# Optimization experiments

Measured on AMD Instinct MI355X. Metric: run time of the kernel, lower is better.

Reference implementation:

```python
import jax, jax.numpy as jnp
import numpy as np

Q_DIM, T_DIM, TOP_M, TEMP = 512, 768, 5, 0.07
B, H, W, K = 8, 64, 64, 128
LN_EPS = 1e-5

def _layernorm(x, g, b):
    mu = jnp.mean(x, axis=-1, keepdims=True)
    var = jnp.mean(jnp.square(x - mu), axis=-1, keepdims=True)
    return (x - mu) * jax.lax.rsqrt(var + LN_EPS) * g + b

def _l2norm(x):
    n = jnp.linalg.norm(x, axis=-1, keepdims=True)
    return x / jnp.maximum(n, 1e-12)

def setup_inputs() -> dict:
    key = jax.random.key(0)
    ks = jax.random.split(key, 12)
    s = lambda d: 1.0 / np.sqrt(d)
    return {
        'visual_features': jax.random.normal(ks[0], (B, H, W, Q_DIM), jnp.float32),
        'text_features': jax.random.normal(ks[1], (B, K, T_DIM), jnp.float32),
        'Wq': jax.random.uniform(ks[2], (Q_DIM, T_DIM), jnp.float32, -s(Q_DIM), s(Q_DIM)),
        'bq': jnp.zeros((T_DIM,), jnp.float32),
        'Wv': jax.random.uniform(ks[3], (T_DIM, Q_DIM), jnp.float32, -s(T_DIM), s(T_DIM)),
        'bv': jnp.zeros((Q_DIM,), jnp.float32),
        'W1': jax.random.uniform(ks[4], (Q_DIM, 4 * Q_DIM), jnp.float32, -s(Q_DIM), s(Q_DIM)),
        'b1': jnp.zeros((4 * Q_DIM,), jnp.float32),
        'W2': jax.random.uniform(ks[5], (4 * Q_DIM, Q_DIM), jnp.float32, -s(4 * Q_DIM), s(4 * Q_DIM)),
        'b2': jnp.zeros((Q_DIM,), jnp.float32),
        'g1': jnp.ones((Q_DIM,), jnp.float32), 'be1': jnp.zeros((Q_DIM,), jnp.float32),
        'g2': jnp.ones((Q_DIM,), jnp.float32), 'be2': jnp.zeros((Q_DIM,), jnp.float32),
    }

def reference(visual_features, text_features, Wq, bq, Wv, bv, W1, b1, W2, b2, g1, be1, g2, be2):
    b, h, w, c = visual_features.shape
    residual = visual_features.reshape(b, h * w, c)
    vis = _layernorm(residual, g1, be1)                      # (B,N,C)
    query = _l2norm(vis @ Wq + bq)                            # (B,N,Ct)
    keyt = _l2norm(text_features)                             # (B,K,Ct)
    value = text_features @ Wv + bv                           # (B,K,C)
    sim = jnp.einsum('bnc,bkc->bnk', query, keyt)             # (B,N,K)
    # top-M sparsification: keep top_m logits, others -> -inf
    top_v = jax.lax.top_k(sim, TOP_M)[0]                      # (B,N,M) sorted desc
    thr = top_v[..., -1:]
    sim = jnp.where(sim >= thr, sim, -jnp.inf)
    attn = jax.nn.softmax(sim / TEMP, axis=-1)
    aligned = jnp.einsum('bnk,bkc->bnc', attn, value)
    fused = residual + aligned
    fused = _layernorm(fused, g2, be2)
    ffn = jax.nn.gelu(fused @ W1 + b1, approximate=False) @ W2 + b2
    out = fused + ffn
    return out.reshape(b, h, w, c)
```

## Files before the change

kernel.cpp:

```cpp
#include <hip/hip_runtime.h>
#include <math.h>

typedef unsigned short u16;
typedef unsigned int   u32;
typedef unsigned long long u64;
typedef __attribute__((ext_vector_type(4))) float f32x4;
typedef __attribute__((ext_vector_type(4))) unsigned int u32x4;
typedef __attribute__((ext_vector_type(8))) _Float16 f16x8;
typedef __attribute__((ext_vector_type(8))) short s16x8;

#define NROWS   32768
#define CDIM    512
#define TDIM    768
#define KKEY    128
#define FFDIM   2048
#define NB      8
#define RPB     4096
#define LN_EPS_ 1e-5f
#define TINV    (1.0f/0.07f)
#define RESCUE_MARGIN 1e-5f

__device__ __forceinline__ u16 f2h(float f){ _Float16 h=(_Float16)f; return __builtin_bit_cast(u16,h); }
__device__ __forceinline__ float h2f(u16 v){ return (float)__builtin_bit_cast(_Float16, v); }
__device__ __forceinline__ unsigned pk2(float a,float b){ return (unsigned)f2h(a)|((unsigned)f2h(b)<<16); }
__device__ __forceinline__ u16 f2b(float f){
  u32 u = __builtin_bit_cast(u32, f);
  u32 r = (u + 0x7fffu + ((u>>16)&1u)) >> 16;
  return (u16)r;
}
__device__ __forceinline__ float b2f(u16 h){ u32 u = ((u32)h)<<16; return __builtin_bit_cast(float, u); }
__device__ __forceinline__ unsigned pkb(float a,float b){ return (unsigned)f2b(a)|((unsigned)f2b(b)<<16); }

__device__ __forceinline__ void gl_lds16(const void* g, void* l){
  __builtin_amdgcn_global_load_lds(
      (const __attribute__((address_space(1))) u32*)g,
      (__attribute__((address_space(3))) u32*)l, 16, 0, 0);
}

__device__ __forceinline__ float fast_exp2(float x){
#if __has_builtin(__builtin_amdgcn_exp2f)
  return __builtin_amdgcn_exp2f(x);
#else
  return exp2f(x);
#endif
}
__device__ __forceinline__ float fast_rcp(float x){
#if __has_builtin(__builtin_amdgcn_rcpf)
  return __builtin_amdgcn_rcpf(x);
#else
  return 1.0f/x;
#endif
}

__device__ __forceinline__ float wsumf(float v){
#pragma unroll
  for(int o=1;o<64;o<<=1) v+=__shfl_xor(v,o);
  return v; }
__device__ __forceinline__ float wmaxf(float v){
#pragma unroll
  for(int o=1;o<64;o<<=1) v=fmaxf(v,__shfl_xor(v,o));
  return v; }
__device__ __forceinline__ double wsumd(double v){
#pragma unroll
  for(int o=1;o<64;o<<=1) v+=__shfl_xor(v,o);
  return v; }
__device__ __forceinline__ double wmaxd(double v){
#pragma unroll
  for(int o=1;o<64;o<<=1){ double t=__shfl_xor(v,o); v = t>v ? t : v; }
  return v; }

__device__ __forceinline__ double blocksumd4(double v, double* red){
  const int lane = threadIdx.x & 63, w = threadIdx.x >> 6;
  v = wsumd(v);
  __syncthreads();
  if (lane==0) red[w] = v;
  __syncthreads();
  return red[0]+red[1]+red[2]+red[3];
}

template<int R, int C, int MODE>
__device__ __forceinline__ void tr_tile(const float* __restrict__ in, void* __restrict__ out,
                                        int bx, int by, float (*tile)[33])
{
  int c0 = bx*32, r0 = by*32;
  int tx = threadIdx.x, ty = threadIdx.y;
#pragma unroll
  for (int i=0;i<4;i++){
    int r = r0 + ty + i*8;
    tile[ty+i*8][tx] = in[(size_t)r*C + c0 + tx];
  }
  __syncthreads();
#pragma unroll
  for (int i=0;i<4;i++){
    int cc = c0 + ty + i*8, rr = r0 + tx;
    float v = tile[tx][ty+i*8];
    if (MODE==1)      ((u16*)out)[(size_t)cc*R + rr] = f2h(v);
    else if (MODE==2) ((u16*)out)[(size_t)cc*R + rr] = f2b(v);
    else              ((float*)out)[(size_t)cc*R + rr] = v;
  }
}

__global__ __launch_bounds__(256) void transpose_all_kernel(
    const float* __restrict__ Wq, const float* __restrict__ W1,
    const float* __restrict__ W2, const float* __restrict__ Wv,
    u16* __restrict__ Wqbt, u16* __restrict__ W116t,
    u16* __restrict__ W216t, float* __restrict__ WvT)
{
  __shared__ float tile[32][33];
  int bid = blockIdx.x;
  if (bid < 384){
    tr_tile<512,768,2>(Wq, Wqbt, bid%24, bid/24, tile);
  } else if (bid < 1408){
    int b = bid-384;  tr_tile<512,2048,1>(W1, W116t, b%64, b/64, tile);
  } else if (bid < 2432){
    int b = bid-1408; tr_tile<2048,512,1>(W2, W216t, b%16, b/16, tile);
  } else {
    int b = bid-2432; tr_tile<768,512,0>(Wv, WvT, b%16, b/16, tile);
  }
}

__global__ __launch_bounds__(256) void keystats_kernel(
    const float* __restrict__ text, const float* __restrict__ bq,
    float* __restrict__ normk, float* __restrict__ crr)
{
  int gw = blockIdx.x*4 + (threadIdx.x>>6);
  int lane = threadIdx.x & 63;
  const float* tr = &text[(size_t)gw*TDIM];
  double ss=0.0, db=0.0;
#pragma unroll
  for (int i=0;i<12;i++){
    float v = tr[lane + 64*i];
    ss += (double)v*(double)v;
    db += (double)bq[lane+64*i]*(double)v;
  }
  ss = wsumd(ss); db = wsumd(db);
  if (lane==0){
    double nk = sqrt(ss); nk = nk>1e-12 ? nk : 1e-12;
    normk[gw] = (float)nk;
    crr[gw]   = (float)db;
  }
}

__global__ __launch_bounds__(256) void ln1_kernel(
    const float* __restrict__ visual, const float* __restrict__ g1, const float* __restrict__ be1,
    u16* __restrict__ visH, u16* __restrict__ visL)
{
  int row = blockIdx.x*4 + (threadIdx.x>>6);
  int lane = threadIdx.x & 63;
  size_t base = (size_t)row*CDIM + lane*8;
  f32x4 a = *(const f32x4*)&visual[base];
  f32x4 c = *(const f32x4*)&visual[base+4];
  float s = a[0]+a[1]+a[2]+a[3]+c[0]+c[1]+c[2]+c[3];
  s = wsumf(s);
  float mu = s * (1.0f/512.0f);
  float q = 0.f;
#pragma unroll
  for (int i=0;i<4;i++){ float d=a[i]-mu; q+=d*d; }
#pragma unroll
  for (int i=0;i<4;i++){ float d=c[i]-mu; q+=d*d; }
  q = wsumf(q);
  float rs = rsqrtf(q*(1.0f/512.0f) + LN_EPS_);
  int cb = lane*8;
  float o[8];
#pragma unroll
  for (int i=0;i<4;i++) o[i]   = (a[i]-mu)*rs*g1[cb+i]   + be1[cb+i];
#pragma unroll
  for (int i=0;i<4;i++) o[4+i] = (c[i]-mu)*rs*g1[cb+4+i] + be1[cb+4+i];
  u16 hh[8];
  float lo[8];
#pragma unroll
  for (int i=0;i<8;i++){ hh[i] = f2b(o[i]); lo[i] = o[i] - b2f(hh[i]); }
  u32x4 hv, lv;
#pragma unroll
  for (int i=0;i<4;i++){
    hv[i] = (u32)hh[2*i] | ((u32)hh[2*i+1]<<16);
    lv[i] = pkb(lo[2*i], lo[2*i+1]);
  }
  *(u32x4*)&visH[base] = hv;
  *(u32x4*)&visL[base] = lv;
}

__global__ __launch_bounds__(256) void gemm_f32_kernel(
    const float* __restrict__ A, const float* __restrict__ Bt, float* __restrict__ C,
    int M, int N, int K, long sA, long sB, long sC)
{
  __shared__ float As[64][17];
  __shared__ float Bs[64][17];
  const int z = blockIdx.z;
  A  += (size_t)z * sA; Bt += (size_t)z * sB; C += (size_t)z * sC;
  const int tid = threadIdx.x;
  const int tx = tid & 15, ty = tid >> 4;
  const int m0 = blockIdx.x*64, n0 = blockIdx.y*64;
  float acc[4][4];
#pragma unroll
  for (int i=0;i<4;i++)
#pragma unroll
    for (int j=0;j<4;j++) acc[i][j]=0.f;
  const int lr = tid >> 2, lc = (tid & 3)*4;
  for (int k0=0; k0<K; k0+=16){
    f32x4 av = *(const f32x4*)&A [(size_t)(m0+lr)*K + k0 + lc];
    f32x4 bv = *(const f32x4*)&Bt[(size_t)(n0+lr)*K + k0 + lc];
#pragma unroll
    for (int i=0;i<4;i++){ As[lr][lc+i]=av[i]; Bs[lr][lc+i]=bv[i]; }
    __syncthreads();
#pragma unroll
    for (int kk=0; kk<16; kk++){
      float a[4], b[4];
#pragma unroll
      for (int i=0;i<4;i++){ a[i]=As[ty*4+i][kk]; b[i]=Bs[tx*4+i][kk]; }
#pragma unroll
      for (int i=0;i<4;i++)
#pragma unroll
        for (int j=0;j<4;j++) acc[i][j] = fmaf(a[i], b[j], acc[i][j]);
    }
    __syncthreads();
  }
#pragma unroll
  for (int i=0;i<4;i++){
    f32x4 o;
#pragma unroll
    for (int j=0;j<4;j++) o[j]=acc[i][j];
    *(f32x4*)&C[(size_t)(m0+ty*4+i)*N + n0 + tx*4] = o;
  }
}

__global__ __launch_bounds__(256) void split_kernel(
    const float* __restrict__ in, u16* __restrict__ hi, u16* __restrict__ lo, int n4)
{
  int i = blockIdx.x*256 + threadIdx.x;
  if (i >= n4) return;
  f32x4 v = *(const f32x4*)&in[i*4];
  u32 hw[2], lw[2];
#pragma unroll
  for (int j=0;j<2;j++){
    u16 h0 = f2b(v[2*j]), h1 = f2b(v[2*j+1]);
    hw[j] = (u32)h0 | ((u32)h1<<16);
    lw[j] = pkb(v[2*j]-b2f(h0), v[2*j+1]-b2f(h1));
  }
  ((u32*)hi)[i*2]   = hw[0]; ((u32*)hi)[i*2+1] = hw[1];
  ((u32*)lo)[i*2]   = lw[0]; ((u32*)lo)[i*2+1] = lw[1];
}

__device__ __forceinline__ float gelu_exact(float v){
  float x  = v*0.70710678118654752440f;
  float ax = fabsf(x);
  float t  = fast_rcp(fmaf(0.3275911f, ax, 1.0f));
  float p  = t*fmaf(t, fmaf(t, fmaf(t, fmaf(t, 1.061405429f, -1.453152027f),
                  1.421413741f), -0.284496736f), 0.254829592f);
  float e  = fast_exp2(ax*ax*(-1.4426950408889634f));
  float y  = 1.0f - p*e;
  float er = (x < 0.0f) ? -y : y;
  return 0.5f*v*(1.0f + er);
}

template<int EPI, int NN, int KK, int NT>
__global__ __launch_bounds__(256) void gemm_f16_kernel(
    const u16* __restrict__ A, const u16* __restrict__ Bt,
    const float* __restrict__ bias,
    float* __restrict__ out_f,
    u16* __restrict__ out_h,
    const u16* __restrict__ add_h)
{
  __shared__ __align__(16) u16 As[2][128*64];
  __shared__ __align__(16) u16 Bs[2][128*64];
  const int tid = threadIdx.x;
  const int lane = tid & 63, w = tid >> 6;
  const int wr = w >> 1, wc = w & 1;
  constexpr int NWG = 256*NT;
  const int wg = blockIdx.x;
  const int b2 = (wg & 7)*(NWG/8) + (wg >> 3);
  const int ntile = b2 % NT, mtile = b2 / NT;
  const int m0 = mtile*128, n0 = ntile*128;
  f32x4 acc[4][4];
#pragma unroll
  for (int i=0;i<4;i++)
#pragma unroll
    for (int j=0;j<4;j++) acc[i][j] = (f32x4)0.f;
  const int lr = lane & 15, lk = (lane >> 4)*8;
  const int c8_sw = ((lane & 7) ^ (lane >> 3))*8;
  const size_t stride32 = (size_t)32*KK;
  const u16* aBase = &A [(size_t)(m0 + w*8 + (lane>>3))*KK + c8_sw];
  const u16* bBase = &Bt[(size_t)(n0 + w*8 + (lane>>3))*KK + c8_sw];

  auto STAGE = [&](int buf, int k0){
#pragma unroll
    for (int i=0;i<4;i++){
      gl_lds16(aBase + i*stride32 + k0, &As[buf][w*512 + i*2048]);
      gl_lds16(bBase + i*stride32 + k0, &Bs[buf][w*512 + i*2048]);
    }
  };

  STAGE(0, 0);
  int cur = 0;
  for (int k0=0; k0<KK; k0+=64){
    if (k0 + 64 < KK){
      STAGE(cur^1, k0+64);
      asm volatile("s_waitcnt vmcnt(8)" ::: "memory");
    } else {
      asm volatile("s_waitcnt vmcnt(0)" ::: "memory");
    }
    __builtin_amdgcn_s_barrier();
#pragma unroll
    for (int kk=0; kk<64; kk+=32){
      s16x8 af[4], bfv[4];
      const int csw = (kk + lk) ^ ((lr & 7) << 3);
#pragma unroll
      for (int mi=0;mi<4;mi++) af[mi]  = *(const s16x8*)&As[cur][(wr*64 + mi*16 + lr)*64 + csw];
#pragma unroll
      for (int ni=0;ni<4;ni++) bfv[ni] = *(const s16x8*)&Bs[cur][(wc*64 + ni*16 + lr)*64 + csw];
#pragma unroll
      for (int mi=0;mi<4;mi++)
#pragma unroll
        for (int ni=0;ni<4;ni++){
          if (EPI == 0)
            acc[mi][ni] = __builtin_amdgcn_mfma_f32_16x16x32_bf16(af[mi], bfv[ni], acc[mi][ni], 0, 0, 0);
          else
            acc[mi][ni] = __builtin_amdgcn_mfma_f32_16x16x32_f16(
                __builtin_bit_cast(f16x8, af[mi]), __builtin_bit_cast(f16x8, bfv[ni]), acc[mi][ni], 0, 0, 0);
        }
    }
    __builtin_amdgcn_s_barrier();
    cur ^= 1;
  }
  const int lr4 = (lane >> 4)*4;
  if (EPI == 0){
    float sq[4][4];
#pragma unroll
    for (int mi=0;mi<4;mi++)
#pragma unroll
      for (int r=0;r<4;r++) sq[mi][r]=0.f;
#pragma unroll
    for (int ni=0;ni<4;ni++){
      float bqv = bias[n0 + wc*64 + ni*16 + lr];
#pragma unroll
      for (int mi=0;mi<4;mi++)
#pragma unroll
        for (int r=0;r<4;r++){
          float v = acc[mi][ni][r] + bqv;
          sq[mi][r] += v*v;
        }
    }
#pragma unroll
    for (int o=1;o<16;o<<=1)
#pragma unroll
      for (int mi=0;mi<4;mi++)
#pragma unroll
        for (int r=0;r<4;r++) sq[mi][r] += __shfl_xor(sq[mi][r], o);
    if ((lane & 15) == 0){
      int part = ntile*2 + wc;
#pragma unroll
      for (int mi=0;mi<4;mi++)
#pragma unroll
        for (int r=0;r<4;r++){
          int row = m0 + wr*64 + mi*16 + lr4 + r;
          out_f[(size_t)row*12 + part] = sq[mi][r];
        }
    }
  } else {
    const int row0 = m0 + wr*64 + lr4;
    const int col0 = n0 + wc*64 + lr;
    float bb[4];
#pragma unroll
    for (int ni=0;ni<4;ni++) bb[ni] = bias[col0 + ni*16];
    if (EPI == 1){
      u16* op = out_h + (size_t)row0*NN + col0;
#pragma unroll
      for (int mi=0;mi<4;mi++)
#pragma unroll
        for (int r=0;r<4;r++)
#pragma unroll
          for (int ni=0;ni<4;ni++)
            op[(size_t)(mi*16+r)*NN + ni*16] = f2h(gelu_exact(acc[mi][ni][r] + bb[ni]));
    } else {
      float* op = out_f + (size_t)row0*NN + col0;
      const u16* rp = add_h + (size_t)row0*NN + col0;
#pragma unroll
      for (int mi=0;mi<4;mi++)
#pragma unroll
        for (int r=0;r<4;r++)
#pragma unroll
          for (int ni=0;ni<4;ni++)
            op[(size_t)(mi*16+r)*NN + ni*16] =
                acc[mi][ni][r] + bb[ni] + h2f(rp[(size_t)(mi*16+r)*NN + ni*16]);
    }
  }
}

__global__ __launch_bounds__(256) void gemm_t_kernel(
    const u16* __restrict__ Ah, const u16* __restrict__ Al,
    const u16* __restrict__ Bh, const u16* __restrict__ Bl,
    float* __restrict__ C)
{
  __shared__ __align__(16) u16 As[2][128*64];
  __shared__ __align__(16) u16 Bs[2][128*64];
  const int tid = threadIdx.x;
  const int lane = tid & 63, w = tid >> 6;
  const int wr = w >> 1, wc = w & 1;
  const int mtile = blockIdx.x;
  const int m0 = mtile*128, z = mtile >> 5;
  f32x4 acc[4][4];
#pragma unroll
  for (int i=0;i<4;i++)
#pragma unroll
    for (int j=0;j<4;j++) acc[i][j] = (f32x4)0.f;
  const int lr = lane & 15, lk = (lane >> 4)*8;
  const int c8_sw = ((lane & 7) ^ (lane >> 3))*8;
  const size_t aOff = (size_t)(m0 + w*8 + (lane>>3))*CDIM + c8_sw;
  const size_t bOff = (size_t)(z*KKEY + w*8 + (lane>>3))*CDIM + c8_sw;
  const size_t stride32 = (size_t)32*CDIM;

  auto STAGE = [&](int buf, int s){
    const int p = s >> 3, k0 = (s & 7) << 6;
    const u16* Ap = (p==2) ? Al : Ah;
    const u16* Bp = (p==1) ? Bl : Bh;
#pragma unroll
    for (int i=0;i<4;i++){
      gl_lds16(Ap + aOff + i*stride32 + k0, &As[buf][w*512 + i*2048]);
      gl_lds16(Bp + bOff + i*stride32 + k0, &Bs[buf][w*512 + i*2048]);
    }
  };

  STAGE(0, 0);
  int cur = 0;
  for (int s=0; s<24; ++s){
    if (s < 23){
      STAGE(cur^1, s+1);
      asm volatile("s_waitcnt vmcnt(8)" ::: "memory");
    } else {
      asm volatile("s_waitcnt vmcnt(0)" ::: "memory");
    }
    __builtin_amdgcn_s_barrier();
#pragma unroll
    for (int kk=0; kk<64; kk+=32){
      s16x8 af[4], bfv[4];
      const int csw = (kk + lk) ^ ((lr & 7) << 3);
#pragma unroll
      for (int mi=0;mi<4;mi++) af[mi]  = *(const s16x8*)&As[cur][(wr*64 + mi*16 + lr)*64 + csw];
#pragma unroll
      for (int ni=0;ni<4;ni++) bfv[ni] = *(const s16x8*)&Bs[cur][(wc*64 + ni*16 + lr)*64 + csw];
#pragma unroll
      for (int mi=0;mi<4;mi++)
#pragma unroll
        for (int ni=0;ni<4;ni++)
          acc[mi][ni] = __builtin_amdgcn_mfma_f32_16x16x32_bf16(af[mi], bfv[ni], acc[mi][ni], 0, 0, 0);
    }
    __builtin_amdgcn_s_barrier();
    cur ^= 1;
  }
  const int lr4 = (lane >> 4)*4;
  const int row0 = m0 + wr*64 + lr4;
  const int col0 = wc*64 + lr;
  float* op = C + (size_t)row0*KKEY + col0;
#pragma unroll
  for (int mi=0;mi<4;mi++)
#pragma unroll
    for (int r=0;r<4;r++)
#pragma unroll
      for (int ni=0;ni<4;ni++)
        op[(size_t)(mi*16+r)*KKEY + ni*16] = acc[mi][ni][r];
}

__global__ __launch_bounds__(256) void rescue_kernel(
    const int* __restrict__ rcnt, const int* __restrict__ rlist,
    const float* __restrict__ visual, const float* __restrict__ text,
    const float* __restrict__ Wq, const float* __restrict__ bq,
    const float* __restrict__ g1, const float* __restrict__ be1,
    const float* __restrict__ g2, const float* __restrict__ be2,
    const float* __restrict__ value, const float* __restrict__ bv,
    u16* __restrict__ fused16)
{
  __shared__ double vis64[512];
  __shared__ double q64[768];
  __shared__ double sims[128];
  __shared__ double pw[128];
  __shared__ double red[4];
  __shared__ double sc2[2];
  __shared__ int klist[128];
  __shared__ int kcount;
  const int tid = threadIdx.x, lane = tid & 63, w = tid >> 6;
  int n = *rcnt; if (n > NROWS) n = NROWS;
  for (int i = blockIdx.x; i < n; i += gridDim.x){
    const int row = rlist[i], b = row >> 12;
    const size_t rb = (size_t)row*CDIM;
    double x0 = (double)visual[rb+tid], x1 = (double)visual[rb+tid+256];
    double s = blocksumd4(x0+x1, red);
    double mu = s*(1.0/512.0);
    double d0 = x0-mu, d1 = x1-mu;
    double var = blocksumd4(d0*d0+d1*d1, red);
    double rs = 1.0/sqrt(var*(1.0/512.0) + 1e-5);
    vis64[tid]     = d0*rs*(double)g1[tid]     + (double)be1[tid];
    vis64[tid+256] = d1*rs*(double)g1[tid+256] + (double)be1[tid+256];
    __syncthreads();
    double qa0=(double)bq[tid], qa1=(double)bq[tid+256], qa2=(double)bq[tid+512];
#pragma unroll 4
    for (int c=0;c<CDIM;c++){
      double v = vis64[c];
      const float* wrow = &Wq[(size_t)c*TDIM];
      qa0 += v*(double)wrow[tid];
      qa1 += v*(double)wrow[tid+256];
      qa2 += v*(double)wrow[tid+512];
    }
    q64[tid]=qa0; q64[tid+256]=qa1; q64[tid+512]=qa2;
    double nq2 = blocksumd4(qa0*qa0+qa1*qa1+qa2*qa2, red);
    double nq = sqrt(nq2); if (nq < 1e-12) nq = 1e-12;
    __syncthreads();
    if (tid < KKEY){
      const float* trow = &text[((size_t)b*KKEY + tid)*TDIM];
      double dot=0.0, nk2=0.0;
#pragma unroll 8
      for (int j=0;j<TDIM;j++){
        double tv = (double)trow[j];
        dot += q64[j]*tv; nk2 += tv*tv;
      }
      double nk = sqrt(nk2); if (nk < 1e-12) nk = 1e-12;
      sims[tid] = dot/(nq*nk);
    }
    __syncthreads();
    if (w == 0){
      double v0=sims[lane], v1=sims[lane+64];
      bool rm0=false, rm1=false;
      double thr=0.0, smax=0.0;
      for (int it=0; it<5; ++it){
        double c0 = rm0 ? -1e300 : v0;
        double c1 = rm1 ? -1e300 : v1;
        double m = wmaxd(c0>c1 ? c0 : c1);
        if (it==0) smax = m;
        thr = m;
        bool h0 = (!rm0) && (v0==m);
        u64 k0 = __ballot(h0);
        if (k0){ if (lane == __ffsll(k0)-1) rm0 = true; }
        else {
          bool h1 = (!rm1) && (v1==m);
          u64 k1 = __ballot(h1);
          if (lane == __ffsll(k1)-1) rm1 = true;
        }
      }
      if (lane==0){ sc2[0]=smax; sc2[1]=thr; kcount=0; }
    }
    __syncthreads();
    const double smax = sc2[0], thr = sc2[1];
    double p = 0.0;
    if (tid < KKEY){
      double sv = sims[tid];
      p = (sv >= thr) ? exp((sv-smax)*(1.0/0.07)) : 0.0;
      pw[tid] = p;
      if (p > 0.0){ int pos = atomicAdd(&kcount, 1); klist[pos] = tid; }
    }
    double Z = blocksumd4(p, red);
    double zi = 1.0/Z;
    __syncthreads();
    double a0=(double)bv[tid], a1=(double)bv[tid+256];
    int kc = kcount;
    for (int ki=0; ki<kc; ++ki){
      int k = klist[ki];
      double wt = pw[k]*zi;
      const float* vr = &value[((size_t)b*KKEY + k)*CDIM];
      a0 += wt*(double)vr[tid];
      a1 += wt*(double)vr[tid+256];
    }
    double f0 = (double)visual[rb+tid]     + a0;
    double f1 = (double)visual[rb+tid+256] + a1;
    double fsum = blocksumd4(f0+f1, red);
    double fmu = fsum*(1.0/512.0);
    double e0=f0-fmu, e1=f1-fmu;
    double fvar = blocksumd4(e0*e0+e1*e1, red);
    double frs = 1.0/sqrt(fvar*(1.0/512.0) + 1e-5);
    fused16[rb+tid]     = f2h((float)(e0*frs*(double)g2[tid]     + (double)be2[tid]));
    fused16[rb+tid+256] = f2h((float)(e1*frs*(double)g2[tid+256] + (double)be2[tid+256]));
    __syncthreads();
  }
}

__global__ __launch_bounds__(256) void attn_ln2_kernel(
    const float* __restrict__ visual,
    const float* __restrict__ tbuf, const float* __restrict__ crr,
    const float* __restrict__ normk, const float* __restrict__ qpart,
    const float* __restrict__ value, const float* __restrict__ bv,
    const float* __restrict__ g2, const float* __restrict__ be2,
    u16* __restrict__ fused16,
    int* __restrict__ rcnt, int* __restrict__ rlist)
{
  const int w = threadIdx.x >> 6, lane = threadIdx.x & 63;
  const int row = blockIdx.x*4 + w;
  const int b = row >> 12;
  float nqp = (lane < 12) ? qpart[(size_t)row*12 + lane] : 0.f;
  float nq2 = wsumf(nqp);
  float nq = fmaxf(sqrtf(nq2), 1e-12f);
  const float* trow = &tbuf[(size_t)row*KKEY];
  float s0 = (trow[lane]    + crr[b*KKEY + lane])    / (nq*normk[b*KKEY + lane]);
  float s1 = (trow[lane+64] + crr[b*KKEY + lane+64]) / (nq*normk[b*KKEY + lane+64]);
  float v0=s0, v1=s1; bool rm0=false, rm1=false;
  float thr=0.f, smax=0.f, m6=0.f;
  for (int it=0; it<6; ++it){
    float c0 = rm0 ? -1e30f : v0;
    float c1 = rm1 ? -1e30f : v1;
    float m = wmaxf(fmaxf(c0,c1));
    if (it==0) smax = m;
    if (it<5){
      thr = m;
      bool h0 = (!rm0) && (v0==m);
      u64 k0 = __ballot(h0);
      if (k0){ if (lane == __ffsll(k0)-1) rm0 = true; }
      else {
        bool h1 = (!rm1) && (v1==m);
        u64 k1 = __ballot(h1);
        if (lane == __ffsll(k1)-1) rm1 = true;
      }
    } else m6 = m;
  }
  if ((thr - m6) < RESCUE_MARGIN){
    if (lane == 0){
      int p = atomicAdd(rcnt, 1);
      rlist[p] = row;
    }
    return;
  }
  float p0 = (s0>=thr) ? expf((s0-smax)*TINV) : 0.f;
  float p1 = (s1>=thr) ? expf((s1-smax)*TINV) : 0.f;
  float Z = wsumf(p0+p1);
  float zi = 1.f/Z;
  float accv[8];
#pragma unroll
  for (int j=0;j<8;j++) accv[j] = bv[lane*8+j];
  u64 mk0 = __ballot(p0>0.f);
  u64 mk1 = __ballot(p1>0.f);
  while (mk0){
    int l = __ffsll(mk0)-1; mk0 &= mk0-1;
    float wt = __shfl(p0, l)*zi;
    const f32x4* vr = (const f32x4*)&value[((size_t)b*KKEY + l)*CDIM + lane*8];
    f32x4 va = vr[0], vb = vr[1];
#pragma unroll
    for (int j=0;j<4;j++){ accv[j] += wt*va[j]; accv[4+j] += wt*vb[j]; }
  }
  while (mk1){
    int l = __ffsll(mk1)-1; mk1 &= mk1-1;
    float wt = __shfl(p1, l)*zi;
    const f32x4* vr = (const f32x4*)&value[((size_t)b*KKEY + l + 64)*CDIM + lane*8];
    f32x4 va = vr[0], vb = vr[1];
#pragma unroll
    for (int j=0;j<4;j++){ accv[j] += wt*va[j]; accv[4+j] += wt*vb[j]; }
  }
  size_t rb = (size_t)row*CDIM + lane*8;
  f32x4 r0v = *(const f32x4*)&visual[rb];
  f32x4 r1v = *(const f32x4*)&visual[rb+4];
  float f[8];
#pragma unroll
  for (int j=0;j<4;j++){ f[j]=r0v[j]+accv[j]; f[4+j]=r1v[j]+accv[4+j]; }
  float fs=0.f;
#pragma unroll
  for (int j=0;j<8;j++) fs += f[j];
  fs = wsumf(fs);
  float fmu = fs*(1.0f/512.0f);
  float fvv=0.f;
#pragma unroll
  for (int j=0;j<8;j++){ float d=f[j]-fmu; fvv+=d*d; }
  fvv = wsumf(fvv);
  float frs = rsqrtf(fvv*(1.0f/512.0f) + LN_EPS_);
  int cb = lane*8;
  f32x4 o0,o1;
#pragma unroll
  for (int j=0;j<4;j++) o0[j] = (f[j]-fmu)*frs*g2[cb+j]     + be2[cb+j];
#pragma unroll
  for (int j=0;j<4;j++) o1[j] = (f[4+j]-fmu)*frs*g2[cb+4+j] + be2[cb+4+j];
  u32x4 hv;
  hv[0]=pk2(o0[0],o0[1]); hv[1]=pk2(o0[2],o0[3]);
  hv[2]=pk2(o1[0],o1[1]); hv[3]=pk2(o1[2],o1[3]);
  *(u32x4*)&fused16[rb] = hv;
}

extern "C" void kernel_launch(void* const* d_in, const int* in_sizes, int n_in,
                              void* d_out, int out_size, void* d_ws, size_t ws_size,
                              hipStream_t stream)
{
  (void)in_sizes; (void)n_in; (void)out_size; (void)ws_size;
  const float* visual = (const float*)d_in[0];
  const float* text   = (const float*)d_in[1];
  const float* Wq     = (const float*)d_in[2];
  const float* bq     = (const float*)d_in[3];
  const float* Wv     = (const float*)d_in[4];
  const float* bv     = (const float*)d_in[5];
  const float* W1     = (const float*)d_in[6];
  const float* b1     = (const float*)d_in[7];
  const float* W2     = (const float*)d_in[8];
  const float* b2     = (const float*)d_in[9];
  const float* g1     = (const float*)d_in[10];
  const float* be1    = (const float*)d_in[11];
  const float* g2     = (const float*)d_in[12];
  const float* be2    = (const float*)d_in[13];
  float* out = (float*)d_out;

  char* ws = (char*)d_ws;
  size_t off = 0;
  auto alloc = [&](size_t bytes)->char*{
    char* p = ws + off; off += (bytes + 255) & ~(size_t)255; return p; };

  u16*    visH   = (u16*)   alloc((size_t)NROWS*CDIM*2);
  u16*    visL   = (u16*)   alloc((size_t)NROWS*CDIM*2);
  u16*    h16    = (u16*)   alloc((size_t)NROWS*FFDIM*2);
  u16*    fused16= (u16*)   alloc((size_t)NROWS*CDIM*2);
  float*  tbuf   = (float*) alloc((size_t)NROWS*KKEY*4);
  float*  Mrt    = (float*) alloc((size_t)NB*KKEY*CDIM*4);
  u16*    MrtH   = (u16*)   alloc((size_t)NB*KKEY*CDIM*2);
  u16*    MrtL   = (u16*)   alloc((size_t)NB*KKEY*CDIM*2);
  float*  value  = (float*) alloc((size_t)NB*KKEY*CDIM*4);
  u16*    Wqbt   = (u16*)   alloc((size_t)TDIM*CDIM*2);
  u16*    W116t  = (u16*)   alloc((size_t)FFDIM*CDIM*2);
  u16*    W216t  = (u16*)   alloc((size_t)CDIM*FFDIM*2);
  float*  WvT    = (float*) alloc((size_t)CDIM*TDIM*4);
  float*  qpart  = (float*) alloc((size_t)NROWS*12*4);
  float*  normk  = (float*) alloc((size_t)NB*KKEY*4);
  float*  crr    = (float*) alloc((size_t)NB*KKEY*4);
  int*    rcnt   = (int*)   alloc(256);
  int*    rlist  = (int*)   alloc((size_t)NROWS*4);

  hipMemsetAsync(rcnt, 0, sizeof(int), stream);

  transpose_all_kernel<<<2816, dim3(32,8), 0, stream>>>(
      Wq, W1, W2, Wv, Wqbt, W116t, W216t, WvT);
  keystats_kernel<<<256, 256, 0, stream>>>(text, bq, normk, crr);
  gemm_f32_kernel<<<dim3(2, 8, 8), 256, 0, stream>>>(
      text, Wq, Mrt, KKEY, CDIM, TDIM, (long)KKEY*TDIM, 0, (long)KKEY*CDIM);
  gemm_f32_kernel<<<dim3(2, 8, 8), 256, 0, stream>>>(
      text, WvT, value, KKEY, CDIM, TDIM, (long)KKEY*TDIM, 0, (long)KKEY*CDIM);
  split_kernel<<<512, 256, 0, stream>>>(Mrt, MrtH, MrtL, NB*KKEY*CDIM/4);
  ln1_kernel<<<NROWS/4, 256, 0, stream>>>(visual, g1, be1, visH, visL);
  gemm_t_kernel<<<256, 256, 0, stream>>>(visH, visL, MrtH, MrtL, tbuf);
  gemm_f16_kernel<0,TDIM,CDIM,6><<<1536, 256, 0, stream>>>(
      visH, Wqbt, bq, qpart, nullptr, nullptr);
  attn_ln2_kernel<<<NROWS/4, 256, 0, stream>>>(
      visual, tbuf, crr, normk, qpart, value, bv, g2, be2,
      fused16, rcnt, rlist);
  rescue_kernel<<<256, 256, 0, stream>>>(
      rcnt, rlist, visual, text, Wq, bq, g1, be1, g2, be2, value, bv, fused16);
  gemm_f16_kernel<1,FFDIM,CDIM,16><<<4096, 256, 0, stream>>>(
      fused16, W116t, b1, nullptr, h16, nullptr);
  gemm_f16_kernel<2,CDIM,FFDIM,4><<<1024, 256, 0, stream>>>(
      h16, W216t, b2, out, nullptr, fused16);
}
```

Baseline: 514.7 us.

## Use 256x256 tile 512-thread GEMM kernel for both FFN matmuls

Adds a new GEMM kernel with 256x256 output tiles, 8 waves per block and an XCD-aware block remap, used for both FFN matmuls in place of the 128x128 tile kernel. The larger tile raises arithmetic intensity per LDS load and cuts global traffic for A and B. The cost is more registers per wave (8x4 accumulators) and one block per CU, so latency hiding is reduced. The FFN2 GEMM now launches only 256 blocks, which may underfill the device.

New measurement: 526.1 us. +2.2%, slower.

```diff
diff --git a/kernel.cpp b/kernel.cpp
--- a/kernel.cpp
+++ b/kernel.cpp
@@ -356,33 +356,101 @@
           out_f[(size_t)row*12 + part] = sq[mi][r];
         }
     }
+  }
+}
+
+template<int EPI, int NN, int KK, int NT>
+__global__ __launch_bounds__(512, 1) void gemm_big_kernel(
+    const u16* __restrict__ A, const u16* __restrict__ Bt,
+    const float* __restrict__ bias,
+    float* __restrict__ out_f,
+    u16* __restrict__ out_h,
+    const u16* __restrict__ add_h)
+{
+  __shared__ __align__(16) u16 As[2][256*64];
+  __shared__ __align__(16) u16 Bs[2][256*64];
+  const int tid = threadIdx.x;
+  const int lane = tid & 63, w = tid >> 6;
+  const int wr = w >> 2, wc = w & 3;
+  constexpr int NWG = 128*NT;
+  const int wg = blockIdx.x;
+  const int b2 = (wg & 7)*(NWG/8) + (wg >> 3);
+  const int ntile = b2 % NT, mtile = b2 / NT;
+  const int m0 = mtile*256, n0 = ntile*256;
+  f32x4 acc[8][4];
+#pragma unroll
+  for (int i=0;i<8;i++)
+#pragma unroll
+    for (int j=0;j<4;j++) acc[i][j] = (f32x4)0.f;
+  const int lr = lane & 15, lk = (lane >> 4)*8;
+  const int c8_sw = ((lane & 7) ^ (lane >> 3))*8;
+  const size_t stride64 = (size_t)64*KK;
+  const u16* aBase = &A [(size_t)(m0 + w*8 + (lane>>3))*KK + c8_sw];
+  const u16* bBase = &Bt[(size_t)(n0 + w*8 + (lane>>3))*KK + c8_sw];
+
+  auto STAGE = [&](int buf, int k0){
+#pragma unroll
+    for (int i=0;i<4;i++){
+      gl_lds16(aBase + i*stride64 + k0, &As[buf][w*512 + i*4096]);
+      gl_lds16(bBase + i*stride64 + k0, &Bs[buf][w*512 + i*4096]);
+    }
+  };
+
+  STAGE(0, 0);
+  int cur = 0;
+  for (int k0=0; k0<KK; k0+=64){
+    if (k0 + 64 < KK){
+      STAGE(cur^1, k0+64);
+      asm volatile("s_waitcnt vmcnt(8)" ::: "memory");
+    } else {
+      asm volatile("s_waitcnt vmcnt(0)" ::: "memory");
+    }
+    __builtin_amdgcn_s_barrier();
+    __builtin_amdgcn_s_setprio(1);
+#pragma unroll
+    for (int kk=0; kk<64; kk+=32){
+      f16x8 af[8], bfv[4];
+      const int csw = (kk + lk) ^ ((lr & 7) << 3);
+#pragma unroll
+      for (int mi=0;mi<8;mi++) af[mi]  = *(const f16x8*)&As[cur][(wr*128 + mi*16 + lr)*64 + csw];
+#pragma unroll
+      for (int ni=0;ni<4;ni++) bfv[ni] = *(const f16x8*)&Bs[cur][(wc*64 + ni*16 + lr)*64 + csw];
+#pragma unroll
+      for (int mi=0;mi<8;mi++)
+#pragma unroll
+        for (int ni=0;ni<4;ni++)
+          acc[mi][ni] = __builtin_amdgcn_mfma_f32_16x16x32_f16(af[mi], bfv[ni], acc[mi][ni], 0, 0, 0);
+    }
+    __builtin_amdgcn_s_setprio(0);
+    __builtin_amdgcn_s_barrier();
+    cur ^= 1;
+  }
+  const int lr4 = (lane >> 4)*4;
+  const int row0 = m0 + wr*128 + lr4;
+  const int col0 = n0 + wc*64 + lr;
+  float bb[4];
+#pragma unroll
+  for (int ni=0;ni<4;ni++) bb[ni] = bias[col0 + ni*16];
+  if (EPI == 1){
+    u16* op = out_h + (size_t)row0*NN + col0;
+#pragma unroll
+    for (int mi=0;mi<8;mi++)
+#pragma unroll
+      for (int r=0;r<4;r++)
+#pragma unroll
+        for (int ni=0;ni<4;ni++)
+          op[(size_t)(mi*16+r)*NN + ni*16] = f2h(gelu_exact(acc[mi][ni][r] + bb[ni]));
   } else {
-    const int row0 = m0 + wr*64 + lr4;
-    const int col0 = n0 + wc*64 + lr;
-    float bb[4];
-#pragma unroll
-    for (int ni=0;ni<4;ni++) bb[ni] = bias[col0 + ni*16];
-    if (EPI == 1){
-      u16* op = out_h + (size_t)row0*NN + col0;
-#pragma unroll
-      for (int mi=0;mi<4;mi++)
-#pragma unroll
-        for (int r=0;r<4;r++)
-#pragma unroll
-          for (int ni=0;ni<4;ni++)
-            op[(size_t)(mi*16+r)*NN + ni*16] = f2h(gelu_exact(acc[mi][ni][r] + bb[ni]));
-    } else {
-      float* op = out_f + (size_t)row0*NN + col0;
-      const u16* rp = add_h + (size_t)row0*NN + col0;
-#pragma unroll
-      for (int mi=0;mi<4;mi++)
-#pragma unroll
-        for (int r=0;r<4;r++)
-#pragma unroll
-          for (int ni=0;ni<4;ni++)
-            op[(size_t)(mi*16+r)*NN + ni*16] =
-                acc[mi][ni][r] + bb[ni] + h2f(rp[(size_t)(mi*16+r)*NN + ni*16]);
-    }
+    float* op = out_f + (size_t)row0*NN + col0;
+    const u16* rp = add_h + (size_t)row0*NN + col0;
+#pragma unroll
+    for (int mi=0;mi<8;mi++)
+#pragma unroll
+      for (int r=0;r<4;r++)
+#pragma unroll
+        for (int ni=0;ni<4;ni++)
+          op[(size_t)(mi*16+r)*NN + ni*16] =
+              acc[mi][ni][r] + bb[ni] + h2f(rp[(size_t)(mi*16+r)*NN + ni*16]);
   }
 }
 
@@ -732,8 +800,8 @@
       fused16, rcnt, rlist);
   rescue_kernel<<<256, 256, 0, stream>>>(
       rcnt, rlist, visual, text, Wq, bq, g1, be1, g2, be2, value, bv, fused16);
-  gemm_f16_kernel<1,FFDIM,CDIM,16><<<4096, 256, 0, stream>>>(
+  gemm_big_kernel<1,FFDIM,CDIM,8><<<1024, 512, 0, stream>>>(
       fused16, W116t, b1, nullptr, h16, nullptr);
-  gemm_f16_kernel<2,CDIM,FFDIM,4><<<1024, 256, 0, stream>>>(
+  gemm_big_kernel<2,CDIM,FFDIM,2><<<256, 512, 0, stream>>>(
       h16, W216t, b2, out, nullptr, fused16);
 }
```

## Enlarge f16 GEMM tiles to 256x256 with 8 waves and prioritized MFMA phases

Applied to the files above, without the earlier changes.

Replaces the 128x128, 4-wave GEMM with a 256x256, 8-wave variant: each wave now computes a 128x64 sub-tile, and B fragments are held across four A sub-steps. The compute loop is split into phases with extra barriers and s_setprio around the MFMA bursts, so waves interleave LDS loads and matrix math. The aim is more reuse per byte loaded and fewer global loads per FLOP for the Q-projection, FFN1 and FFN2 GEMMs. In exchange, LDS use doubles to 128KB and register pressure grows, which forces one block per CU. The grids also get small: the FFN2 GEMM launches only 256 blocks, which may underfill the device.

After: 553.7 us. 1.08x slower.

```diff
diff --git a/kernel.cpp b/kernel.cpp
--- a/kernel.cpp
+++ b/kernel.cpp
@@ -254,39 +254,39 @@
 }
 
 template<int EPI, int NN, int KK, int NT>
-__global__ __launch_bounds__(256) void gemm_f16_kernel(
+__global__ __launch_bounds__(512, 1) void gemm_big_kernel(
     const u16* __restrict__ A, const u16* __restrict__ Bt,
     const float* __restrict__ bias,
     float* __restrict__ out_f,
     u16* __restrict__ out_h,
     const u16* __restrict__ add_h)
 {
-  __shared__ __align__(16) u16 As[2][128*64];
-  __shared__ __align__(16) u16 Bs[2][128*64];
+  __shared__ __align__(16) u16 As[2][256*64];
+  __shared__ __align__(16) u16 Bs[2][256*64];
   const int tid = threadIdx.x;
   const int lane = tid & 63, w = tid >> 6;
-  const int wr = w >> 1, wc = w & 1;
-  constexpr int NWG = 256*NT;
+  const int wr = w >> 2, wc = w & 3;
+  constexpr int NWG = 128*NT;
   const int wg = blockIdx.x;
   const int b2 = (wg & 7)*(NWG/8) + (wg >> 3);
   const int ntile = b2 % NT, mtile = b2 / NT;
-  const int m0 = mtile*128, n0 = ntile*128;
-  f32x4 acc[4][4];
-#pragma unroll
-  for (int i=0;i<4;i++)
+  const int m0 = mtile*256, n0 = ntile*256;
+  f32x4 acc[8][4];
+#pragma unroll
+  for (int i=0;i<8;i++)
 #pragma unroll
     for (int j=0;j<4;j++) acc[i][j] = (f32x4)0.f;
   const int lr = lane & 15, lk = (lane >> 4)*8;
   const int c8_sw = ((lane & 7) ^ (lane >> 3))*8;
-  const size_t stride32 = (size_t)32*KK;
+  const size_t stride64 = (size_t)64*KK;
   const u16* aBase = &A [(size_t)(m0 + w*8 + (lane>>3))*KK + c8_sw];
   const u16* bBase = &Bt[(size_t)(n0 + w*8 + (lane>>3))*KK + c8_sw];
 
   auto STAGE = [&](int buf, int k0){
 #pragma unroll
     for (int i=0;i<4;i++){
-      gl_lds16(aBase + i*stride32 + k0, &As[buf][w*512 + i*2048]);
-      gl_lds16(bBase + i*stride32 + k0, &Bs[buf][w*512 + i*2048]);
+      gl_lds16(aBase + i*stride64 + k0, &As[buf][w*512 + i*4096]);
+      gl_lds16(bBase + i*stride64 + k0, &Bs[buf][w*512 + i*4096]);
     }
   };
 
@@ -300,40 +300,57 @@
       asm volatile("s_waitcnt vmcnt(0)" ::: "memory");
     }
     __builtin_amdgcn_s_barrier();
-#pragma unroll
-    for (int kk=0; kk<64; kk+=32){
-      s16x8 af[4], bfv[4];
-      const int csw = (kk + lk) ^ ((lr & 7) << 3);
-#pragma unroll
-      for (int mi=0;mi<4;mi++) af[mi]  = *(const s16x8*)&As[cur][(wr*64 + mi*16 + lr)*64 + csw];
-#pragma unroll
-      for (int ni=0;ni<4;ni++) bfv[ni] = *(const s16x8*)&Bs[cur][(wc*64 + ni*16 + lr)*64 + csw];
-#pragma unroll
-      for (int mi=0;mi<4;mi++)
-#pragma unroll
-        for (int ni=0;ni<4;ni++){
-          if (EPI == 0)
-            acc[mi][ni] = __builtin_amdgcn_mfma_f32_16x16x32_bf16(af[mi], bfv[ni], acc[mi][ni], 0, 0, 0);
-          else
-            acc[mi][ni] = __builtin_amdgcn_mfma_f32_16x16x32_f16(
-                __builtin_bit_cast(f16x8, af[mi]), __builtin_bit_cast(f16x8, bfv[ni]), acc[mi][ni], 0, 0, 0);
+    s16x8 bfv[4][2];
+#pragma unroll
+    for (int ni=0;ni<4;ni++)
+#pragma unroll
+      for (int kh=0;kh<2;kh++){
+        const int csw = (kh*32 + lk) ^ ((lr & 7) << 3);
+        bfv[ni][kh] = *(const s16x8*)&Bs[cur][(wc*64 + ni*16 + lr)*64 + csw];
+      }
+#pragma unroll
+    for (int q=0;q<4;q++){
+      s16x8 af[2][2];
+#pragma unroll
+      for (int m2=0;m2<2;m2++)
+#pragma unroll
+        for (int kh=0;kh<2;kh++){
+          const int csw = (kh*32 + lk) ^ ((lr & 7) << 3);
+          af[m2][kh] = *(const s16x8*)&As[cur][(wr*128 + (q*2+m2)*16 + lr)*64 + csw];
         }
-    }
-    __builtin_amdgcn_s_barrier();
+      __builtin_amdgcn_s_barrier();
+      __builtin_amdgcn_s_setprio(1);
+#pragma unroll
+      for (int m2=0;m2<2;m2++)
+#pragma unroll
+        for (int ni=0;ni<4;ni++)
+#pragma unroll
+          for (int kh=0;kh<2;kh++){
+            if (EPI == 0)
+              acc[q*2+m2][ni] = __builtin_amdgcn_mfma_f32_16x16x32_bf16(
+                  af[m2][kh], bfv[ni][kh], acc[q*2+m2][ni], 0, 0, 0);
+            else
+              acc[q*2+m2][ni] = __builtin_amdgcn_mfma_f32_16x16x32_f16(
+                  __builtin_bit_cast(f16x8, af[m2][kh]),
+                  __builtin_bit_cast(f16x8, bfv[ni][kh]), acc[q*2+m2][ni], 0, 0, 0);
+          }
+      __builtin_amdgcn_s_setprio(0);
+      __builtin_amdgcn_s_barrier();
+    }
     cur ^= 1;
   }
   const int lr4 = (lane >> 4)*4;
   if (EPI == 0){
-    float sq[4][4];
-#pragma unroll
-    for (int mi=0;mi<4;mi++)
+    float sq[8][4];
+#pragma unroll
+    for (int mi=0;mi<8;mi++)
 #pragma unroll
       for (int r=0;r<4;r++) sq[mi][r]=0.f;
 #pragma unroll
     for (int ni=0;ni<4;ni++){
       float bqv = bias[n0 + wc*64 + ni*16 + lr];
 #pragma unroll
-      for (int mi=0;mi<4;mi++)
+      for (int mi=0;mi<8;mi++)
 #pragma unroll
         for (int r=0;r<4;r++){
           float v = acc[mi][ni][r] + bqv;
@@ -343,21 +360,21 @@
 #pragma unroll
     for (int o=1;o<16;o<<=1)
 #pragma unroll
-      for (int mi=0;mi<4;mi++)
+      for (int mi=0;mi<8;mi++)
 #pragma unroll
         for (int r=0;r<4;r++) sq[mi][r] += __shfl_xor(sq[mi][r], o);
     if ((lane & 15) == 0){
-      int part = ntile*2 + wc;
-#pragma unroll
-      for (int mi=0;mi<4;mi++)
+      int part = ntile*4 + wc;
+#pragma unroll
+      for (int mi=0;mi<8;mi++)
 #pragma unroll
         for (int r=0;r<4;r++){
-          int row = m0 + wr*64 + mi*16 + lr4 + r;
+          int row = m0 + wr*128 + mi*16 + lr4 + r;
           out_f[(size_t)row*12 + part] = sq[mi][r];
         }
     }
   } else {
-    const int row0 = m0 + wr*64 + lr4;
+    const int row0 = m0 + wr*128 + lr4;
     const int col0 = n0 + wc*64 + lr;
     float bb[4];
 #pragma unroll
@@ -365,7 +382,7 @@
     if (EPI == 1){
       u16* op = out_h + (size_t)row0*NN + col0;
 #pragma unroll
-      for (int mi=0;mi<4;mi++)
+      for (int mi=0;mi<8;mi++)
 #pragma unroll
         for (int r=0;r<4;r++)
 #pragma unroll
@@ -375,7 +392,7 @@
       float* op = out_f + (size_t)row0*NN + col0;
       const u16* rp = add_h + (size_t)row0*NN + col0;
 #pragma unroll
-      for (int mi=0;mi<4;mi++)
+      for (int mi=0;mi<8;mi++)
 #pragma unroll
         for (int r=0;r<4;r++)
 #pragma unroll
@@ -725,15 +742,15 @@
   split_kernel<<<512, 256, 0, stream>>>(Mrt, MrtH, MrtL, NB*KKEY*CDIM/4);
   ln1_kernel<<<NROWS/4, 256, 0, stream>>>(visual, g1, be1, visH, visL);
   gemm_t_kernel<<<256, 256, 0, stream>>>(visH, visL, MrtH, MrtL, tbuf);
-  gemm_f16_kernel<0,TDIM,CDIM,6><<<1536, 256, 0, stream>>>(
+  gemm_big_kernel<0,TDIM,CDIM,3><<<384, 512, 0, stream>>>(
       visH, Wqbt, bq, qpart, nullptr, nullptr);
   attn_ln2_kernel<<<NROWS/4, 256, 0, stream>>>(
       visual, tbuf, crr, normk, qpart, value, bv, g2, be2,
       fused16, rcnt, rlist);
   rescue_kernel<<<256, 256, 0, stream>>>(
       rcnt, rlist, visual, text, Wq, bq, g1, be1, g2, be2, value, bv, fused16);
-  gemm_f16_kernel<1,FFDIM,CDIM,16><<<4096, 256, 0, stream>>>(
+  gemm_big_kernel<1,FFDIM,CDIM,8><<<1024, 512, 0, stream>>>(
       fused16, W116t, b1, nullptr, h16, nullptr);
-  gemm_f16_kernel<2,CDIM,FFDIM,4><<<1024, 256, 0, stream>>>(
+  gemm_big_kernel<2,CDIM,FFDIM,2><<<256, 512, 0, stream>>>(
       h16, W216t, b2, out, nullptr, fused16);
 }
```

## Split similarity GEMM passes across blocks and fuse text GEMMs with hi/lo split

Applied to the files above, without the earlier changes.

The three hi/lo precision passes of the similarity GEMM now run as separate blocks (grid y=3), each writing its own partial buffer, and the attention kernel sums the three partials. This raises the GEMM from 256 blocks to 768 so more of the GPU is occupied. The cost is extra partial-buffer traffic, and the buffers alias the FFN hidden buffer h16, which is not yet in use at that point. The two small text GEMMs and the split kernel are merged into one launch that writes the bf16 hi/lo halves directly, removing two launches and an fp32 intermediate.

New measurement: 458.6 us. 10.9% less time.

```diff
diff --git a/kernel.cpp b/kernel.cpp
--- a/kernel.cpp
+++ b/kernel.cpp
@@ -180,14 +180,18 @@
   *(u32x4*)&visL[base] = lv;
 }
 
-__global__ __launch_bounds__(256) void gemm_f32_kernel(
-    const float* __restrict__ A, const float* __restrict__ Bt, float* __restrict__ C,
-    int M, int N, int K, long sA, long sB, long sC)
+__global__ __launch_bounds__(256) void gemm_txt_kernel(
+    const float* __restrict__ text, const float* __restrict__ Wq,
+    const float* __restrict__ WvT,
+    u16* __restrict__ MrtH, u16* __restrict__ MrtL, float* __restrict__ value)
 {
   __shared__ float As[64][17];
   __shared__ float Bs[64][17];
-  const int z = blockIdx.z;
-  A  += (size_t)z * sA; Bt += (size_t)z * sB; C += (size_t)z * sC;
+  const int zz = blockIdx.z;
+  const bool isV = zz >= 8;
+  const int z = isV ? zz-8 : zz;
+  const float* A  = text + (size_t)z*KKEY*TDIM;
+  const float* Bt = isV ? WvT : Wq;
   const int tid = threadIdx.x;
   const int tx = tid & 15, ty = tid >> 4;
   const int m0 = blockIdx.x*64, n0 = blockIdx.y*64;
@@ -197,9 +201,9 @@
 #pragma unroll
     for (int j=0;j<4;j++) acc[i][j]=0.f;
   const int lr = tid >> 2, lc = (tid & 3)*4;
-  for (int k0=0; k0<K; k0+=16){
-    f32x4 av = *(const f32x4*)&A [(size_t)(m0+lr)*K + k0 + lc];
-    f32x4 bv = *(const f32x4*)&Bt[(size_t)(n0+lr)*K + k0 + lc];
+  for (int k0=0; k0<TDIM; k0+=16){
+    f32x4 av = *(const f32x4*)&A [(size_t)(m0+lr)*TDIM + k0 + lc];
+    f32x4 bv = *(const f32x4*)&Bt[(size_t)(n0+lr)*TDIM + k0 + lc];
 #pragma unroll
     for (int i=0;i<4;i++){ As[lr][lc+i]=av[i]; Bs[lr][lc+i]=bv[i]; }
     __syncthreads();
@@ -217,28 +221,27 @@
   }
 #pragma unroll
   for (int i=0;i<4;i++){
-    f32x4 o;
-#pragma unroll
-    for (int j=0;j<4;j++) o[j]=acc[i][j];
-    *(f32x4*)&C[(size_t)(m0+ty*4+i)*N + n0 + tx*4] = o;
-  }
-}
-
-__global__ __launch_bounds__(256) void split_kernel(
-    const float* __restrict__ in, u16* __restrict__ hi, u16* __restrict__ lo, int n4)
-{
-  int i = blockIdx.x*256 + threadIdx.x;
-  if (i >= n4) return;
-  f32x4 v = *(const f32x4*)&in[i*4];
-  u32 hw[2], lw[2];
-#pragma unroll
-  for (int j=0;j<2;j++){
-    u16 h0 = f2b(v[2*j]), h1 = f2b(v[2*j+1]);
-    hw[j] = (u32)h0 | ((u32)h1<<16);
-    lw[j] = pkb(v[2*j]-b2f(h0), v[2*j+1]-b2f(h1));
-  }
-  ((u32*)hi)[i*2]   = hw[0]; ((u32*)hi)[i*2+1] = hw[1];
-  ((u32*)lo)[i*2]   = lw[0]; ((u32*)lo)[i*2+1] = lw[1];
+    size_t idx = ((size_t)z*KKEY + m0 + ty*4 + i)*CDIM + n0 + tx*4;
+    if (isV){
+      f32x4 o;
+#pragma unroll
+      for (int j=0;j<4;j++) o[j]=acc[i][j];
+      *(f32x4*)&value[idx] = o;
+    } else {
+      u16 hh[4]; u16 ll[4];
+#pragma unroll
+      for (int j=0;j<4;j++){
+        float v = acc[i][j];
+        u16 h = f2b(v);
+        hh[j] = h;
+        ll[j] = f2b(v - b2f(h));
+      }
+      ((u32*)&MrtH[idx])[0] = (u32)hh[0] | ((u32)hh[1]<<16);
+      ((u32*)&MrtH[idx])[1] = (u32)hh[2] | ((u32)hh[3]<<16);
+      ((u32*)&MrtL[idx])[0] = (u32)ll[0] | ((u32)ll[1]<<16);
+      ((u32*)&MrtL[idx])[1] = (u32)ll[2] | ((u32)ll[3]<<16);
+    }
+  }
 }
 
 __device__ __forceinline__ float gelu_exact(float v){
@@ -397,7 +400,10 @@
   const int lane = tid & 63, w = tid >> 6;
   const int wr = w >> 1, wc = w & 1;
   const int mtile = blockIdx.x;
+  const int p = blockIdx.y;
   const int m0 = mtile*128, z = mtile >> 5;
+  const u16* Ap = (p==2) ? Al : Ah;
+  const u16* Bp = (p==1) ? Bl : Bh;
   f32x4 acc[4][4];
 #pragma unroll
   for (int i=0;i<4;i++)
@@ -410,9 +416,7 @@
   const size_t stride32 = (size_t)32*CDIM;
 
   auto STAGE = [&](int buf, int s){
-    const int p = s >> 3, k0 = (s & 7) << 6;
-    const u16* Ap = (p==2) ? Al : Ah;
-    const u16* Bp = (p==1) ? Bl : Bh;
+    const int k0 = s << 6;
 #pragma unroll
     for (int i=0;i<4;i++){
       gl_lds16(Ap + aOff + i*stride32 + k0, &As[buf][w*512 + i*2048]);
@@ -422,8 +426,8 @@
 
   STAGE(0, 0);
   int cur = 0;
-  for (int s=0; s<24; ++s){
-    if (s < 23){
+  for (int s=0; s<8; ++s){
+    if (s < 7){
       STAGE(cur^1, s+1);
       asm volatile("s_waitcnt vmcnt(8)" ::: "memory");
     } else {
@@ -450,7 +454,7 @@
   const int lr4 = (lane >> 4)*4;
   const int row0 = m0 + wr*64 + lr4;
   const int col0 = wc*64 + lr;
-  float* op = C + (size_t)row0*KKEY + col0;
+  float* op = C + (size_t)p*NROWS*KKEY + (size_t)row0*KKEY + col0;
 #pragma unroll
   for (int mi=0;mi<4;mi++)
 #pragma unroll
@@ -586,9 +590,13 @@
   float nqp = (lane < 12) ? qpart[(size_t)row*12 + lane] : 0.f;
   float nq2 = wsumf(nqp);
   float nq = fmaxf(sqrtf(nq2), 1e-12f);
-  const float* trow = &tbuf[(size_t)row*KKEY];
-  float s0 = (trow[lane]    + crr[b*KKEY + lane])    / (nq*normk[b*KKEY + lane]);
-  float s1 = (trow[lane+64] + crr[b*KKEY + lane+64]) / (nq*normk[b*KKEY + lane+64]);
+  const float* t0 = &tbuf[(size_t)row*KKEY];
+  const float* t1 = t0 + (size_t)NROWS*KKEY;
+  const float* t2 = t1 + (size_t)NROWS*KKEY;
+  float ta = t0[lane]    + t1[lane]    + t2[lane];
+  float tb = t0[lane+64] + t1[lane+64] + t2[lane+64];
+  float s0 = (ta + crr[b*KKEY + lane])    / (nq*normk[b*KKEY + lane]);
+  float s1 = (tb + crr[b*KKEY + lane+64]) / (nq*normk[b*KKEY + lane+64]);
   float v0=s0, v1=s1; bool rm0=false, rm1=false;
   float thr=0.f, smax=0.f, m6=0.f;
   for (int it=0; it<6; ++it){
@@ -698,8 +706,6 @@
   u16*    visL   = (u16*)   alloc((size_t)NROWS*CDIM*2);
   u16*    h16    = (u16*)   alloc((size_t)NROWS*FFDIM*2);
   u16*    fused16= (u16*)   alloc((size_t)NROWS*CDIM*2);
-  float*  tbuf   = (float*) alloc((size_t)NROWS*KKEY*4);
-  float*  Mrt    = (float*) alloc((size_t)NB*KKEY*CDIM*4);
   u16*    MrtH   = (u16*)   alloc((size_t)NB*KKEY*CDIM*2);
   u16*    MrtL   = (u16*)   alloc((size_t)NB*KKEY*CDIM*2);
   float*  value  = (float*) alloc((size_t)NB*KKEY*CDIM*4);
@@ -712,19 +718,17 @@
   float*  crr    = (float*) alloc((size_t)NB*KKEY*4);
   int*    rcnt   = (int*)   alloc(256);
   int*    rlist  = (int*)   alloc((size_t)NROWS*4);
+  float*  tbuf   = (float*)h16;
 
   hipMemsetAsync(rcnt, 0, sizeof(int), stream);
 
   transpose_all_kernel<<<2816, dim3(32,8), 0, stream>>>(
       Wq, W1, W2, Wv, Wqbt, W116t, W216t, WvT);
   keystats_kernel<<<256, 256, 0, stream>>>(text, bq, normk, crr);
-  gemm_f32_kernel<<<dim3(2, 8, 8), 256, 0, stream>>>(
-      text, Wq, Mrt, KKEY, CDIM, TDIM, (long)KKEY*TDIM, 0, (long)KKEY*CDIM);
-  gemm_f32_kernel<<<dim3(2, 8, 8), 256, 0, stream>>>(
-      text, WvT, value, KKEY, CDIM, TDIM, (long)KKEY*TDIM, 0, (long)KKEY*CDIM);
-  split_kernel<<<512, 256, 0, stream>>>(Mrt, MrtH, MrtL, NB*KKEY*CDIM/4);
+  gemm_txt_kernel<<<dim3(2, 8, 16), 256, 0, stream>>>(
+      text, Wq, WvT, MrtH, MrtL, value);
   ln1_kernel<<<NROWS/4, 256, 0, stream>>>(visual, g1, be1, visH, visL);
-  gemm_t_kernel<<<256, 256, 0, stream>>>(visH, visL, MrtH, MrtL, tbuf);
+  gemm_t_kernel<<<dim3(256, 3), 256, 0, stream>>>(visH, visL, MrtH, MrtL, tbuf);
   gemm_f16_kernel<0,TDIM,CDIM,6><<<1536, 256, 0, stream>>>(
       visH, Wqbt, bq, qpart, nullptr, nullptr);
   attn_ln2_kernel<<<NROWS/4, 256, 0, stream>>>(
```
